# Kernel tuning notes

Hardware: AMD Instinct MI355X
Metric: run time of the kernel (lower is better)

Reference implementation:

```python
import jax, jax.numpy as jnp
import numpy as np

N = 100000   # num nodes
E = 1600000  # num edges
D = 64       # feature / hidden dim (irreps_in == hidden_dim)
SCALE = D ** -0.5


def setup_inputs() -> dict:
    key = jax.random.key(0)
    ks = jax.random.split(key, 6)
    x = jax.random.normal(ks[0], (N, D), dtype=jnp.float32)
    edge_index = jax.random.randint(ks[1], (2, E), 0, N, dtype=jnp.int32)
    std = D ** -0.5
    Wq = jax.random.normal(ks[2], (D, D), dtype=jnp.float32) * std
    Wk = jax.random.normal(ks[3], (D, D), dtype=jnp.float32) * std
    Wv = jax.random.normal(ks[4], (D, D), dtype=jnp.float32) * std
    Wo = jax.random.normal(ks[5], (D, D), dtype=jnp.float32) * std
    return {"x": x, "edge_index": edge_index, "Wq": Wq, "Wk": Wk, "Wv": Wv, "Wo": Wo}


def reference(x, edge_index, Wq, Wk, Wv, Wo):
    # Per-receiver variable-length attention over incoming neighbors.
    # Mathematically identical to the torch module's degree-bucketed SDPA
    # (softmax over each node's neighbor set), without padding buffers.
    sender, receiver = edge_index[0], edge_index[1]
    Q = x @ Wq  # [N, D]
    K = x @ Wk
    V = x @ Wv
    # per-edge logits: <Q[receiver], K[sender]> * scale
    s = jnp.einsum('ed,ed->e', Q[receiver], K[sender]) * SCALE  # [E]
    # numerically stable segment softmax over receiver groups
    m = jax.ops.segment_max(s, receiver, num_segments=N)  # -inf for empty segments
    m_safe = jnp.where(jnp.isfinite(m), m, 0.0)
    p = jnp.exp(s - m_safe[receiver])  # [E]
    denom = jax.ops.segment_sum(p, receiver, num_segments=N)  # [N]
    num = jax.ops.segment_sum(p[:, None] * V[sender], receiver, num_segments=N)  # [N, D]
    # zero-degree nodes get out = 0 (matches torch: skipped buckets + nan_to_num)
    out = jnp.where(denom[:, None] > 0,
                    num / jnp.maximum(denom, 1e-30)[:, None],
                    0.0)
    return x + out @ Wo
```

## Files before the change

kernel.cpp:

```cpp
#include <hip/hip_runtime.h>
#include <hip/hip_bf16.h>

#define DIM 64
#define SCALE 0.125f
#define BINSH 5
#define NPB 32
#define NBKT 8
#define SCAP 192
#define LLCAP (NBKT * SCAP)
#define CHUNK 16384
#define MAXBINS 3200

static __device__ __forceinline__ unsigned int pack2bf(float a, float b) {
    unsigned int ua = __float_as_uint(a), ub = __float_as_uint(b);
    ua += 0x7fffu + ((ua >> 16) & 1u);
    ub += 0x7fffu + ((ub >> 16) & 1u);
    return (ua >> 16) | (ub & 0xffff0000u);
}
static __device__ __forceinline__ float2 unpack2bf(unsigned int u) {
    return make_float2(__uint_as_float(u << 16), __uint_as_float(u & 0xffff0000u));
}

__global__ __launch_bounds__(1024) void k_prep(const int* __restrict__ send,
                                               const int* __restrict__ recv,
                                               const float* __restrict__ Wv,
                                               const float* __restrict__ Wo,
                                               float* __restrict__ Wvo,
                                               int* __restrict__ binCur,
                                               unsigned int* __restrict__ ebuf,
                                               int E, int NBK) {
    __shared__ __align__(16) float smem[8192];
    int* hist = (int*)smem;
    int* lcur = hist + MAXBINS;
    int tid = threadIdx.x;

    if (blockIdx.x == 0) {
        float* av = smem;
        float* bo = smem + 4096;
        ((float4*)av)[tid] = ((const float4*)Wv)[tid];
        ((float4*)bo)[tid] = ((const float4*)Wo)[tid];
        __syncthreads();
        int r = tid >> 4, c0 = (tid & 15) * 4;
        float acc[4] = {0.f, 0.f, 0.f, 0.f};
        for (int k = 0; k < 64; k++) {
            float a = av[r * 64 + k];
#pragma unroll
            for (int j = 0; j < 4; j++) acc[j] = fmaf(a, bo[k * 64 + c0 + j], acc[j]);
        }
#pragma unroll
        for (int j = 0; j < 4; j++) Wvo[r * 64 + c0 + j] = acc[j];
        __syncthreads();
    }

    int bucket = blockIdx.x & (NBKT - 1);
    int base = blockIdx.x * CHUNK;
    int lim = min(base + CHUNK, E);

    for (int i = tid; i < NBK; i += 1024) hist[i] = 0;
    __syncthreads();
    for (int i = base + tid; i < lim; i += 1024)
        atomicAdd(&hist[recv[i] >> BINSH], 1);
    __syncthreads();
    for (int i = tid; i < NBK; i += 1024) {
        int h = hist[i];
        lcur[i] = h ? atomicAdd(&binCur[i * NBKT + bucket], h) : 0;
    }
    __syncthreads();
    for (int i = base + tid; i < lim; i += 1024) {
        int r = recv[i];
        int b = r >> BINSH;
        int p = atomicAdd(&lcur[b], 1);
        if (p < SCAP)
            ebuf[((size_t)b * NBKT + bucket) * SCAP + p] =
                (unsigned)send[i] | ((unsigned)(r & (NPB - 1)) << 17);
    }
}

__global__ __launch_bounds__(256) void k_qkv(const float* __restrict__ x,
                                             const float* __restrict__ Wq,
                                             const float* __restrict__ Wk,
                                             const float* __restrict__ Wvo,
                                             float* __restrict__ Q,
                                             unsigned int* __restrict__ KVb,
                                             int N, int nchunk) {
    __shared__ __align__(16) float ws[64 * 64];
    __shared__ __align__(16) float xs[4][64 * 64];
    int tid = threadIdx.x;
    int wv = tid >> 6;
    int lane = tid & 63;
    int m = blockIdx.x / nchunk;
    int cb = blockIdx.x % nchunk;
    const float* W = (m == 0) ? Wq : ((m == 1) ? Wk : Wvo);

    for (int i = tid; i < 1024; i += 256) ((float4*)ws)[i] = ((const float4*)W)[i];
    __syncthreads();

    int base = cb * 256 + wv * 64;
    if (base < N) {
        float* xw = xs[wv];
#pragma unroll
        for (int c4 = 0; c4 < 16; c4++) {
            float4 v = make_float4(0.f, 0.f, 0.f, 0.f);
            if (base + lane < N) v = ((const float4*)x)[(size_t)(base + lane) * 16 + c4];
            xw[(c4 * 4 + 0) * 64 + lane] = v.x;
            xw[(c4 * 4 + 1) * 64 + lane] = v.y;
            xw[(c4 * 4 + 2) * 64 + lane] = v.z;
            xw[(c4 * 4 + 3) * 64 + lane] = v.w;
        }
        asm volatile("s_waitcnt lgkmcnt(0)" ::: "memory");

        int lr = lane >> 3;
        int lc = lane & 7;
        const float* xp = xw + lr * 8;
        const float* wp = ws + lc * 8;

        float acc[8][8];
#pragma unroll
        for (int i = 0; i < 8; i++)
#pragma unroll
            for (int j = 0; j < 8; j++) acc[i][j] = 0.f;

        float4 xa = *(const float4*)(xp);
        float4 xb = *(const float4*)(xp + 4);
        float4 wa = *(const float4*)(wp);
        float4 wb = *(const float4*)(wp + 4);
#pragma unroll 4
        for (int k = 0; k < 64; k++) {
            float4 xan, xbn, wan, wbn;
            if (k < 63) {
                xan = *(const float4*)(xp + (k + 1) * 64);
                xbn = *(const float4*)(xp + (k + 1) * 64 + 4);
                wan = *(const float4*)(wp + (k + 1) * 64);
                wbn = *(const float4*)(wp + (k + 1) * 64 + 4);
            }
            float xv[8] = {xa.x, xa.y, xa.z, xa.w, xb.x, xb.y, xb.z, xb.w};
            float wc[8] = {wa.x, wa.y, wa.z, wa.w, wb.x, wb.y, wb.z, wb.w};
#pragma unroll
            for (int i = 0; i < 8; i++)
#pragma unroll
                for (int j = 0; j < 8; j++)
                    acc[i][j] = fmaf(xv[i], wc[j], acc[i][j]);
            xa = xan; xb = xbn; wa = wan; wb = wbn;
        }

#pragma unroll
        for (int i = 0; i < 8; i++) {
            int row = base + lr * 8 + i;
            if (row < N) {
                if (m == 0) {
                    float* dst = &Q[(size_t)row * 64 + lc * 8];
                    ((float4*)dst)[0] = make_float4(acc[i][0], acc[i][1], acc[i][2], acc[i][3]);
                    ((float4*)dst)[1] = make_float4(acc[i][4], acc[i][5], acc[i][6], acc[i][7]);
                } else {
                    unsigned int* dst = &KVb[(size_t)row * 64 + (m - 1) * 32 + lc * 4];
                    uint4 pk;
                    pk.x = pack2bf(acc[i][0], acc[i][1]);
                    pk.y = pack2bf(acc[i][2], acc[i][3]);
                    pk.z = pack2bf(acc[i][4], acc[i][5]);
                    pk.w = pack2bf(acc[i][6], acc[i][7]);
                    *((uint4*)dst) = pk;
                }
            }
        }
    }
}

__global__ __launch_bounds__(256) void k_attn(const float* __restrict__ Q,
                                              const unsigned int* __restrict__ KVb,
                                              const float* __restrict__ x,
                                              const int* __restrict__ binCur,
                                              const unsigned int* __restrict__ ebuf,
                                              float* __restrict__ out, int N) {
    __shared__ unsigned int llist[LLCAP];
    __shared__ int ldeg[NPB], lofs[NPB + 1], lcur[NPB];
    __shared__ int segc[NBKT];
    int tid = threadIdx.x;
    int wv = tid >> 6;
    int lane = tid & 63;
    int g = lane >> 3;
    int sub = lane & 7;

    int j = blockIdx.x;
    const unsigned int* ebin = ebuf + (size_t)j * NBKT * SCAP;

    if (tid < NBKT) segc[tid] = min(binCur[j * NBKT + tid], SCAP);
    if (tid < NPB) ldeg[tid] = 0;
    __syncthreads();

    for (int s = 0; s < NBKT; s++) {
        int c = segc[s];
        for (int i = tid; i < c; i += 256)
            atomicAdd(&ldeg[(ebin[s * SCAP + i] >> 17) & (NPB - 1)], 1);
    }
    __syncthreads();

    if (wv == 0 && lane < NPB) {
        int d = ldeg[lane];
        int s = d;
        for (int o = 1; o < NPB; o <<= 1) {
            int t = __shfl_up(s, o, NPB);
            if ((lane & (NPB - 1)) >= o) s += t;
        }
        lofs[lane + 1] = s;
        lcur[lane] = s - d;
        if (lane == 0) lofs[0] = 0;
    }
    __syncthreads();

    for (int s = 0; s < NBKT; s++) {
        int c = segc[s];
        for (int i = tid; i < c; i += 256) {
            unsigned int u = ebin[s * SCAP + i];
            int n = (u >> 17) & (NPB - 1);
            int p = atomicAdd(&lcur[n], 1);
            llist[p] = u & 0x1FFFFu;
        }
    }
    __syncthreads();

    for (int n = wv; n < NPB; n += 4) {
        int r = (j << BINSH) + n;
        if (r >= N) break;
        int start = lofs[n];
        int end = lofs[n + 1];
        float4 qa = *((const float4*)&Q[(size_t)r * 64 + sub * 8]);
        float4 qb = *((const float4*)&Q[(size_t)r * 64 + sub * 8 + 4]);
        float q[8] = {qa.x, qa.y, qa.z, qa.w, qb.x, qb.y, qb.z, qb.w};
        float acc[8] = {0.f, 0.f, 0.f, 0.f, 0.f, 0.f, 0.f, 0.f};
        float dpart = 0.f;

        int eA = start + g;
        bool vA = eA < end;
        unsigned int sA = vA ? llist[eA] : 0u;
        uint4 kA = *((const uint4*)&KVb[(size_t)sA * 64 + sub * 4]);
        uint4 uA = *((const uint4*)&KVb[(size_t)sA * 64 + 32 + sub * 4]);
        int eB = start + 8 + g;
        bool vB = eB < end;
        unsigned int sB = vB ? llist[eB] : 0u;
        uint4 kB = *((const uint4*)&KVb[(size_t)sB * 64 + sub * 4]);
        uint4 uB = *((const uint4*)&KVb[(size_t)sB * 64 + 32 + sub * 4]);
        int eC = start + 16 + g;
        bool vC = eC < end;
        unsigned int sC = vC ? llist[eC] : 0u;
        uint4 kC = *((const uint4*)&KVb[(size_t)sC * 64 + sub * 4]);
        uint4 uC = *((const uint4*)&KVb[(size_t)sC * 64 + 32 + sub * 4]);

        for (int bb = start; bb < end; bb += 8) {
            int eD = bb + 24 + g;
            bool vD = eD < end;
            unsigned int sD = vD ? llist[eD] : 0u;
            uint4 kD = *((const uint4*)&KVb[(size_t)sD * 64 + sub * 4]);
            uint4 uD = *((const uint4*)&KVb[(size_t)sD * 64 + 32 + sub * 4]);

            float2 k01 = unpack2bf(kA.x), k23 = unpack2bf(kA.y);
            float2 k45 = unpack2bf(kA.z), k67 = unpack2bf(kA.w);
            float dot = q[0] * k01.x + q[1] * k01.y + q[2] * k23.x + q[3] * k23.y
                      + q[4] * k45.x + q[5] * k45.y + q[6] * k67.x + q[7] * k67.y;
            dot += __shfl_xor(dot, 1);
            dot += __shfl_xor(dot, 2);
            dot += __shfl_xor(dot, 4);
            float w = vA ? __expf(dot * SCALE) : 0.f;

            float2 v01 = unpack2bf(uA.x), v23 = unpack2bf(uA.y);
            float2 v45 = unpack2bf(uA.z), v67 = unpack2bf(uA.w);
            acc[0] = fmaf(w, v01.x, acc[0]);
            acc[1] = fmaf(w, v01.y, acc[1]);
            acc[2] = fmaf(w, v23.x, acc[2]);
            acc[3] = fmaf(w, v23.y, acc[3]);
            acc[4] = fmaf(w, v45.x, acc[4]);
            acc[5] = fmaf(w, v45.y, acc[5]);
            acc[6] = fmaf(w, v67.x, acc[6]);
            acc[7] = fmaf(w, v67.y, acc[7]);
            dpart += w;

            kA = kB; uA = uB; vA = vB;
            kB = kC; uB = uC; vB = vC;
            kC = kD; uC = uD; vC = vD;
        }

        dpart += __shfl_xor(dpart, 8); dpart += __shfl_xor(dpart, 16); dpart += __shfl_xor(dpart, 32);
#pragma unroll
        for (int jj = 0; jj < 8; jj++) {
            acc[jj] += __shfl_xor(acc[jj], 8);
            acc[jj] += __shfl_xor(acc[jj], 16);
            acc[jj] += __shfl_xor(acc[jj], 32);
        }

        float inv = (dpart > 0.f) ? (1.0f / dpart) : 0.f;

        if (g == 0) {
            float4 xa = *((const float4*)&x[(size_t)r * 64 + sub * 8]);
            float4 xb = *((const float4*)&x[(size_t)r * 64 + sub * 8 + 4]);
            float4 oa = make_float4(fmaf(acc[0], inv, xa.x), fmaf(acc[1], inv, xa.y),
                                    fmaf(acc[2], inv, xa.z), fmaf(acc[3], inv, xa.w));
            float4 ob = make_float4(fmaf(acc[4], inv, xb.x), fmaf(acc[5], inv, xb.y),
                                    fmaf(acc[6], inv, xb.z), fmaf(acc[7], inv, xb.w));
            *((float4*)&out[(size_t)r * 64 + sub * 8]) = oa;
            *((float4*)&out[(size_t)r * 64 + sub * 8 + 4]) = ob;
        }
    }
}


extern "C" void kernel_launch(void* const* d_in, const int* in_sizes, int n_in,
                              void* d_out, int out_size, void* d_ws, size_t ws_size,
                              hipStream_t stream) {
    const float* x  = (const float*)d_in[0];
    const int* edge = (const int*)d_in[1];
    const float* Wq = (const float*)d_in[2];
    const float* Wk = (const float*)d_in[3];
    const float* Wv = (const float*)d_in[4];
    const float* Wo = (const float*)d_in[5];
    float* out = (float*)d_out;

    int N = in_sizes[0] / DIM;
    int E = in_sizes[1] / 2;
    int NBK = (N + NPB - 1) >> BINSH;

    char* p = (char*)d_ws;
    auto cv = [&](size_t bytes) {
        char* r = p;
        p += ((bytes + 255) / 256) * 256;
        return r;
    };
    float*        Q      = (float*)cv((size_t)N * 64 * 4);
    unsigned int* KVb    = (unsigned int*)cv((size_t)N * 64 * 4);
    float*        Wvo    = (float*)cv(64 * 64 * 4);
    int*          binCur = (int*)cv((size_t)NBK * NBKT * 4);
    unsigned int* ebuf   = (unsigned int*)cv((size_t)NBK * NBKT * SCAP * 4);
    (void)ws_size; (void)n_in; (void)out_size;

    const int* send = edge;
    const int* recv = edge + E;

    hipMemsetAsync(binCur, 0, (size_t)NBK * NBKT * 4, stream);
    k_prep<<<(E + CHUNK - 1) / CHUNK, 1024, 0, stream>>>(send, recv, Wv, Wo, Wvo,
                                                         binCur, ebuf, E, NBK);
    int nchunk = (N + 255) / 256;
    k_qkv<<<3 * nchunk, 256, 0, stream>>>(x, Wq, Wk, Wvo, Q, KVb, N, nchunk);
    k_attn<<<NBK, 256, 0, stream>>>(Q, KVb, x, binCur, ebuf, out, N);
}
```

Baseline: 239.4 us.

## Process flat edge list per block with shared-memory atomic accumulation per receiver

Replaces the per-block counting sort of edges by receiver (degree histogram, prefix scan, scatter) with a flat concatenation of the bin segments. Waves now walk edge groups uniformly and accumulate weighted V rows and denominators into shared memory with atomics, indexed by receiver. Q rows for the block are staged in LDS. This removes two atomic passes and the per-node load imbalance across waves, at the cost of many LDS float atomics per edge and a cap of 768 edges per block, down from 1536.

```diff
diff --git a/kernel.cpp b/kernel.cpp
--- a/kernel.cpp
+++ b/kernel.cpp
@@ -7,7 +7,8 @@
 #define NPB 32
 #define NBKT 8
 #define SCAP 192
-#define LLCAP (NBKT * SCAP)
+#define LLCAP 768
+#define QS_S 68
 #define CHUNK 16384
 #define MAXBINS 3200
 
@@ -172,8 +173,11 @@
                                               const unsigned int* __restrict__ ebuf,
                                               float* __restrict__ out, int N) {
     __shared__ unsigned int llist[LLCAP];
-    __shared__ int ldeg[NPB], lofs[NPB + 1], lcur[NPB];
-    __shared__ int segc[NBKT];
+    __shared__ __align__(16) float qs[NPB * QS_S];
+    __shared__ __align__(16) float accw[NPB * QS_S];
+    __shared__ float dsum[NPB];
+    __shared__ int pref[NBKT + 1];
+
     int tid = threadIdx.x;
     int wv = tid >> 6;
     int lane = tid & 63;
@@ -183,120 +187,113 @@
     int j = blockIdx.x;
     const unsigned int* ebin = ebuf + (size_t)j * NBKT * SCAP;
 
-    if (tid < NBKT) segc[tid] = min(binCur[j * NBKT + tid], SCAP);
-    if (tid < NPB) ldeg[tid] = 0;
-    __syncthreads();
-
-    for (int s = 0; s < NBKT; s++) {
-        int c = segc[s];
-        for (int i = tid; i < c; i += 256)
-            atomicAdd(&ldeg[(ebin[s * SCAP + i] >> 17) & (NPB - 1)], 1);
-    }
-    __syncthreads();
-
-    if (wv == 0 && lane < NPB) {
-        int d = ldeg[lane];
-        int s = d;
-        for (int o = 1; o < NPB; o <<= 1) {
-            int t = __shfl_up(s, o, NPB);
-            if ((lane & (NPB - 1)) >= o) s += t;
-        }
-        lofs[lane + 1] = s;
-        lcur[lane] = s - d;
-        if (lane == 0) lofs[0] = 0;
-    }
-    __syncthreads();
-
-    for (int s = 0; s < NBKT; s++) {
-        int c = segc[s];
-        for (int i = tid; i < c; i += 256) {
-            unsigned int u = ebin[s * SCAP + i];
-            int n = (u >> 17) & (NPB - 1);
-            int p = atomicAdd(&lcur[n], 1);
-            llist[p] = u & 0x1FFFFu;
-        }
-    }
-    __syncthreads();
-
-    for (int n = wv; n < NPB; n += 4) {
+    for (int i = tid; i < NPB * 16; i += 256) {
+        int n = i >> 4, c4 = i & 15;
         int r = (j << BINSH) + n;
-        if (r >= N) break;
-        int start = lofs[n];
-        int end = lofs[n + 1];
-        float4 qa = *((const float4*)&Q[(size_t)r * 64 + sub * 8]);
-        float4 qb = *((const float4*)&Q[(size_t)r * 64 + sub * 8 + 4]);
-        float q[8] = {qa.x, qa.y, qa.z, qa.w, qb.x, qb.y, qb.z, qb.w};
-        float acc[8] = {0.f, 0.f, 0.f, 0.f, 0.f, 0.f, 0.f, 0.f};
-        float dpart = 0.f;
-
-        int eA = start + g;
-        bool vA = eA < end;
-        unsigned int sA = vA ? llist[eA] : 0u;
-        uint4 kA = *((const uint4*)&KVb[(size_t)sA * 64 + sub * 4]);
-        uint4 uA = *((const uint4*)&KVb[(size_t)sA * 64 + 32 + sub * 4]);
-        int eB = start + 8 + g;
-        bool vB = eB < end;
-        unsigned int sB = vB ? llist[eB] : 0u;
-        uint4 kB = *((const uint4*)&KVb[(size_t)sB * 64 + sub * 4]);
-        uint4 uB = *((const uint4*)&KVb[(size_t)sB * 64 + 32 + sub * 4]);
-        int eC = start + 16 + g;
-        bool vC = eC < end;
-        unsigned int sC = vC ? llist[eC] : 0u;
+        float4 v = make_float4(0.f, 0.f, 0.f, 0.f);
+        if (r < N) v = ((const float4*)Q)[(size_t)r * 16 + c4];
+        *(float4*)&qs[n * QS_S + c4 * 4] = v;
+    }
+    for (int i = tid; i < NPB * (QS_S / 4); i += 256)
+        *(float4*)&accw[i * 4] = make_float4(0.f, 0.f, 0.f, 0.f);
+    if (tid < NPB) dsum[tid] = 0.f;
+    if (tid < NBKT) pref[tid + 1] = min(binCur[j * NBKT + tid], SCAP);
+    __syncthreads();
+    if (tid == 0) {
+        int a = 0;
+        pref[0] = 0;
+#pragma unroll
+        for (int s = 0; s < NBKT; s++) {
+            a += pref[s + 1];
+            if (a > LLCAP) a = LLCAP;
+            pref[s + 1] = a;
+        }
+    }
+    __syncthreads();
+    int cnt = pref[NBKT];
+
+    for (int f = tid; f < cnt; f += 256) {
+        int s = 0;
+        while (f >= pref[s + 1]) s++;
+        llist[f] = ebin[s * SCAP + (f - pref[s])];
+    }
+    __syncthreads();
+
+    int nb = (cnt + 7) >> 3;
+
+    unsigned wA, wB, wC;
+    bool vA, vB, vC;
+    uint4 kA, uA, kB, uB;
+    {
+        int f = (wv << 3) + g;          vA = f < cnt; wA = vA ? llist[f] : 0u;
+        f = ((wv + 4) << 3) + g;        vB = f < cnt; wB = vB ? llist[f] : 0u;
+        f = ((wv + 8) << 3) + g;        vC = f < cnt; wC = vC ? llist[f] : 0u;
+    }
+    {
+        unsigned sA = wA & 0x1FFFFu, sB = wB & 0x1FFFFu;
+        kA = *((const uint4*)&KVb[(size_t)sA * 64 + sub * 4]);
+        uA = *((const uint4*)&KVb[(size_t)sA * 64 + 32 + sub * 4]);
+        kB = *((const uint4*)&KVb[(size_t)sB * 64 + sub * 4]);
+        uB = *((const uint4*)&KVb[(size_t)sB * 64 + 32 + sub * 4]);
+    }
+
+    for (int b = wv; b < nb; b += 4) {
+        int fD = ((b + 12) << 3) + g;
+        bool vD = fD < cnt;
+        unsigned wD = vD ? llist[fD] : 0u;
+        unsigned sC = wC & 0x1FFFFu;
         uint4 kC = *((const uint4*)&KVb[(size_t)sC * 64 + sub * 4]);
         uint4 uC = *((const uint4*)&KVb[(size_t)sC * 64 + 32 + sub * 4]);
 
-        for (int bb = start; bb < end; bb += 8) {
-            int eD = bb + 24 + g;
-            bool vD = eD < end;
-            unsigned int sD = vD ? llist[eD] : 0u;
-            uint4 kD = *((const uint4*)&KVb[(size_t)sD * 64 + sub * 4]);
-            uint4 uD = *((const uint4*)&KVb[(size_t)sD * 64 + 32 + sub * 4]);
-
-            float2 k01 = unpack2bf(kA.x), k23 = unpack2bf(kA.y);
-            float2 k45 = unpack2bf(kA.z), k67 = unpack2bf(kA.w);
-            float dot = q[0] * k01.x + q[1] * k01.y + q[2] * k23.x + q[3] * k23.y
-                      + q[4] * k45.x + q[5] * k45.y + q[6] * k67.x + q[7] * k67.y;
-            dot += __shfl_xor(dot, 1);
-            dot += __shfl_xor(dot, 2);
-            dot += __shfl_xor(dot, 4);
-            float w = vA ? __expf(dot * SCALE) : 0.f;
-
-            float2 v01 = unpack2bf(uA.x), v23 = unpack2bf(uA.y);
-            float2 v45 = unpack2bf(uA.z), v67 = unpack2bf(uA.w);
-            acc[0] = fmaf(w, v01.x, acc[0]);
-            acc[1] = fmaf(w, v01.y, acc[1]);
-            acc[2] = fmaf(w, v23.x, acc[2]);
-            acc[3] = fmaf(w, v23.y, acc[3]);
-            acc[4] = fmaf(w, v45.x, acc[4]);
-            acc[5] = fmaf(w, v45.y, acc[5]);
-            acc[6] = fmaf(w, v67.x, acc[6]);
-            acc[7] = fmaf(w, v67.y, acc[7]);
-            dpart += w;
-
-            kA = kB; uA = uB; vA = vB;
-            kB = kC; uB = uC; vB = vC;
-            kC = kD; uC = uD; vC = vD;
-        }
-
-        dpart += __shfl_xor(dpart, 8); dpart += __shfl_xor(dpart, 16); dpart += __shfl_xor(dpart, 32);
-#pragma unroll
-        for (int jj = 0; jj < 8; jj++) {
-            acc[jj] += __shfl_xor(acc[jj], 8);
-            acc[jj] += __shfl_xor(acc[jj], 16);
-            acc[jj] += __shfl_xor(acc[jj], 32);
-        }
-
-        float inv = (dpart > 0.f) ? (1.0f / dpart) : 0.f;
-
-        if (g == 0) {
-            float4 xa = *((const float4*)&x[(size_t)r * 64 + sub * 8]);
-            float4 xb = *((const float4*)&x[(size_t)r * 64 + sub * 8 + 4]);
-            float4 oa = make_float4(fmaf(acc[0], inv, xa.x), fmaf(acc[1], inv, xa.y),
-                                    fmaf(acc[2], inv, xa.z), fmaf(acc[3], inv, xa.w));
-            float4 ob = make_float4(fmaf(acc[4], inv, xb.x), fmaf(acc[5], inv, xb.y),
-                                    fmaf(acc[6], inv, xb.z), fmaf(acc[7], inv, xb.w));
-            *((float4*)&out[(size_t)r * 64 + sub * 8]) = oa;
-            *((float4*)&out[(size_t)r * 64 + sub * 8 + 4]) = ob;
+        int nA = (wA >> 17) & (NPB - 1);
+        const float* qp = &qs[nA * QS_S + sub * 8];
+        float4 qa = *(const float4*)qp;
+        float4 qb = *(const float4*)(qp + 4);
+        float2 k01 = unpack2bf(kA.x), k23 = unpack2bf(kA.y);
+        float2 k45 = unpack2bf(kA.z), k67 = unpack2bf(kA.w);
+        float dot = qa.x * k01.x + qa.y * k01.y + qa.z * k23.x + qa.w * k23.y
+                  + qb.x * k45.x + qb.y * k45.y + qb.z * k67.x + qb.w * k67.y;
+        dot += __shfl_xor(dot, 1);
+        dot += __shfl_xor(dot, 2);
+        dot += __shfl_xor(dot, 4);
+        float w = vA ? __expf(dot * SCALE) : 0.f;
+
+        float2 v01 = unpack2bf(uA.x), v23 = unpack2bf(uA.y);
+        float2 v45 = unpack2bf(uA.z), v67 = unpack2bf(uA.w);
+        float* ap = &accw[nA * QS_S + sub * 8];
+        atomicAdd(ap + 0, w * v01.x);
+        atomicAdd(ap + 1, w * v01.y);
+        atomicAdd(ap + 2, w * v23.x);
+        atomicAdd(ap + 3, w * v23.y);
+        atomicAdd(ap + 4, w * v45.x);
+        atomicAdd(ap + 5, w * v45.y);
+        atomicAdd(ap + 6, w * v67.x);
+        atomicAdd(ap + 7, w * v67.y);
+        if (sub == 0) atomicAdd(&dsum[nA], w);
+
+        wA = wB; vA = vB; kA = kB; uA = uB;
+        wB = wC; vB = vC; kB = kC; uB = uC;
+        wC = wD; vC = vD;
+    }
+    __syncthreads();
+
+    {
+        int n = tid >> 3;
+        int d0 = (tid & 7) * 8;
+        int r = (j << BINSH) + n;
+        if (r < N) {
+            float den = dsum[n];
+            float inv = (den > 0.f) ? (1.0f / den) : 0.f;
+            float4 a1 = *(const float4*)&accw[n * QS_S + d0];
+            float4 a2 = *(const float4*)&accw[n * QS_S + d0 + 4];
+            float4 xa = *((const float4*)&x[(size_t)r * 64 + d0]);
+            float4 xb = *((const float4*)&x[(size_t)r * 64 + d0 + 4]);
+            float4 oa = make_float4(fmaf(a1.x, inv, xa.x), fmaf(a1.y, inv, xa.y),
+                                    fmaf(a1.z, inv, xa.z), fmaf(a1.w, inv, xa.w));
+            float4 ob = make_float4(fmaf(a2.x, inv, xb.x), fmaf(a2.y, inv, xb.y),
+                                    fmaf(a2.z, inv, xb.z), fmaf(a2.w, inv, xb.w));
+            *((float4*)&out[(size_t)r * 64 + d0]) = oa;
+            *((float4*)&out[(size_t)r * 64 + d0 + 4]) = ob;
         }
     }
 }
```

New measurement: 741.3 us. 210% more time.

## Flatten per-wave edge batches across nodes to keep gather prefetch pipeline continuous

Applied to the files above, without the earlier changes.

Each wave now builds a queue of 8-edge batches covering all of its assigned nodes, and runs one continuous software-pipelined loop over that queue, flushing accumulators whenever the node changes. Before, the prefetch pipeline restarted for every node. Q rows are staged in shared memory up front, the bin scans become flat loops, the local list shrinks to 768 entries with clamping, and zero-degree nodes are written as plain x copies. The intent is to remove pipeline ramp-up and drain bubbles at node boundaries and to hide gather latency better. The cost is extra shared memory, per-batch shared-memory lookups, and the risk of silently dropping edges when a bin exceeds the list or queue capacity.

```diff
diff --git a/kernel.cpp b/kernel.cpp
--- a/kernel.cpp
+++ b/kernel.cpp
@@ -7,7 +7,9 @@
 #define NPB 32
 #define NBKT 8
 #define SCAP 192
-#define LLCAP (NBKT * SCAP)
+#define LLCAP 768
+#define QS_S 68
+#define WQCAP 112
 #define CHUNK 16384
 #define MAXBINS 3200
 
@@ -172,8 +174,12 @@
                                               const unsigned int* __restrict__ ebuf,
                                               float* __restrict__ out, int N) {
     __shared__ unsigned int llist[LLCAP];
+    __shared__ __align__(16) float qs[NPB * QS_S];
     __shared__ int ldeg[NPB], lofs[NPB + 1], lcur[NPB];
     __shared__ int segc[NBKT];
+    __shared__ unsigned short wbat[4][WQCAP];
+    __shared__ int wnbs[4];
+
     int tid = threadIdx.x;
     int wv = tid >> 6;
     int lane = tid & 63;
@@ -183,112 +189,100 @@
     int j = blockIdx.x;
     const unsigned int* ebin = ebuf + (size_t)j * NBKT * SCAP;
 
+    for (int i = tid; i < NPB * 16; i += 256) {
+        int n = i >> 4, c4 = i & 15;
+        int r = (j << BINSH) + n;
+        float4 v = make_float4(0.f, 0.f, 0.f, 0.f);
+        if (r < N) v = ((const float4*)Q)[(size_t)r * 16 + c4];
+        *(float4*)&qs[n * QS_S + c4 * 4] = v;
+    }
     if (tid < NBKT) segc[tid] = min(binCur[j * NBKT + tid], SCAP);
     if (tid < NPB) ldeg[tid] = 0;
     __syncthreads();
 
-    for (int s = 0; s < NBKT; s++) {
-        int c = segc[s];
-        for (int i = tid; i < c; i += 256)
-            atomicAdd(&ldeg[(ebin[s * SCAP + i] >> 17) & (NPB - 1)], 1);
+    for (int i = tid; i < NBKT * SCAP; i += 256) {
+        int s = i / SCAP;
+        if ((i - s * SCAP) < segc[s])
+            atomicAdd(&ldeg[(ebin[i] >> 17) & (NPB - 1)], 1);
     }
     __syncthreads();
 
     if (wv == 0 && lane < NPB) {
         int d = ldeg[lane];
-        int s = d;
+        int ssum = d;
         for (int o = 1; o < NPB; o <<= 1) {
-            int t = __shfl_up(s, o, NPB);
-            if ((lane & (NPB - 1)) >= o) s += t;
-        }
-        lofs[lane + 1] = s;
-        lcur[lane] = s - d;
+            int t = __shfl_up(ssum, o, NPB);
+            if (lane >= o) ssum += t;
+        }
+        lofs[lane + 1] = min(ssum, LLCAP);
+        lcur[lane] = min(ssum - d, LLCAP);
         if (lane == 0) lofs[0] = 0;
     }
     __syncthreads();
 
-    for (int s = 0; s < NBKT; s++) {
-        int c = segc[s];
-        for (int i = tid; i < c; i += 256) {
-            unsigned int u = ebin[s * SCAP + i];
+    for (int i = tid; i < NBKT * SCAP; i += 256) {
+        int s = i / SCAP;
+        if ((i - s * SCAP) < segc[s]) {
+            unsigned u = ebin[i];
             int n = (u >> 17) & (NPB - 1);
             int p = atomicAdd(&lcur[n], 1);
-            llist[p] = u & 0x1FFFFu;
-        }
-    }
-    __syncthreads();
-
-    for (int n = wv; n < NPB; n += 4) {
-        int r = (j << BINSH) + n;
-        if (r >= N) break;
-        int start = lofs[n];
-        int end = lofs[n + 1];
-        float4 qa = *((const float4*)&Q[(size_t)r * 64 + sub * 8]);
-        float4 qb = *((const float4*)&Q[(size_t)r * 64 + sub * 8 + 4]);
-        float q[8] = {qa.x, qa.y, qa.z, qa.w, qb.x, qb.y, qb.z, qb.w};
-        float acc[8] = {0.f, 0.f, 0.f, 0.f, 0.f, 0.f, 0.f, 0.f};
-        float dpart = 0.f;
-
-        int eA = start + g;
-        bool vA = eA < end;
-        unsigned int sA = vA ? llist[eA] : 0u;
-        uint4 kA = *((const uint4*)&KVb[(size_t)sA * 64 + sub * 4]);
-        uint4 uA = *((const uint4*)&KVb[(size_t)sA * 64 + 32 + sub * 4]);
-        int eB = start + 8 + g;
-        bool vB = eB < end;
-        unsigned int sB = vB ? llist[eB] : 0u;
-        uint4 kB = *((const uint4*)&KVb[(size_t)sB * 64 + sub * 4]);
-        uint4 uB = *((const uint4*)&KVb[(size_t)sB * 64 + 32 + sub * 4]);
-        int eC = start + 16 + g;
-        bool vC = eC < end;
-        unsigned int sC = vC ? llist[eC] : 0u;
-        uint4 kC = *((const uint4*)&KVb[(size_t)sC * 64 + sub * 4]);
-        uint4 uC = *((const uint4*)&KVb[(size_t)sC * 64 + 32 + sub * 4]);
-
-        for (int bb = start; bb < end; bb += 8) {
-            int eD = bb + 24 + g;
-            bool vD = eD < end;
-            unsigned int sD = vD ? llist[eD] : 0u;
-            uint4 kD = *((const uint4*)&KVb[(size_t)sD * 64 + sub * 4]);
-            uint4 uD = *((const uint4*)&KVb[(size_t)sD * 64 + 32 + sub * 4]);
-
-            float2 k01 = unpack2bf(kA.x), k23 = unpack2bf(kA.y);
-            float2 k45 = unpack2bf(kA.z), k67 = unpack2bf(kA.w);
-            float dot = q[0] * k01.x + q[1] * k01.y + q[2] * k23.x + q[3] * k23.y
-                      + q[4] * k45.x + q[5] * k45.y + q[6] * k67.x + q[7] * k67.y;
-            dot += __shfl_xor(dot, 1);
-            dot += __shfl_xor(dot, 2);
-            dot += __shfl_xor(dot, 4);
-            float w = vA ? __expf(dot * SCALE) : 0.f;
-
-            float2 v01 = unpack2bf(uA.x), v23 = unpack2bf(uA.y);
-            float2 v45 = unpack2bf(uA.z), v67 = unpack2bf(uA.w);
-            acc[0] = fmaf(w, v01.x, acc[0]);
-            acc[1] = fmaf(w, v01.y, acc[1]);
-            acc[2] = fmaf(w, v23.x, acc[2]);
-            acc[3] = fmaf(w, v23.y, acc[3]);
-            acc[4] = fmaf(w, v45.x, acc[4]);
-            acc[5] = fmaf(w, v45.y, acc[5]);
-            acc[6] = fmaf(w, v67.x, acc[6]);
-            acc[7] = fmaf(w, v67.y, acc[7]);
-            dpart += w;
-
-            kA = kB; uA = uB; vA = vB;
-            kB = kC; uB = uC; vB = vC;
-            kC = kD; uC = uD; vC = vD;
-        }
-
-        dpart += __shfl_xor(dpart, 8); dpart += __shfl_xor(dpart, 16); dpart += __shfl_xor(dpart, 32);
+            if (p < LLCAP) llist[p] = u & 0x1FFFFu;
+        }
+    }
+    if (lane == 0) {
+        int c = 0;
+        for (int i = 0; i < 8; i++) {
+            int n = wv + 4 * i;
+            int deg = lofs[n + 1] - lofs[n];
+            int nb = (deg + 7) >> 3;
+            for (int t = 0; t < nb && c < WQCAP; t++)
+                wbat[wv][c++] = (unsigned short)(n | (t << 5));
+        }
+        wnbs[wv] = c;
+    }
+    __syncthreads();
+
+    int wnb = wnbs[wv];
+    const unsigned short* wq = wbat[wv];
+
+    int n0 = 0, n1 = 0;
+    bool v0 = false, v1 = false;
+    unsigned s0 = 0, s1 = 0;
+    if (0 < wnb) {
+        unsigned short w = wq[0];
+        n0 = w & 31; int t = w >> 5;
+        int e = lofs[n0] + (t << 3) + g;
+        v0 = e < lofs[n0 + 1];
+        s0 = v0 ? llist[e] : 0u;
+    }
+    if (1 < wnb) {
+        unsigned short w = wq[1];
+        n1 = w & 31; int t = w >> 5;
+        int e = lofs[n1] + (t << 3) + g;
+        v1 = e < lofs[n1 + 1];
+        s1 = v1 ? llist[e] : 0u;
+    }
+    uint4 k0 = *((const uint4*)&KVb[(size_t)s0 * 64 + sub * 4]);
+    uint4 u0 = *((const uint4*)&KVb[(size_t)s0 * 64 + 32 + sub * 4]);
+    uint4 k1 = *((const uint4*)&KVb[(size_t)s1 * 64 + sub * 4]);
+    uint4 u1 = *((const uint4*)&KVb[(size_t)s1 * 64 + 32 + sub * 4]);
+
+    int curn = -1;
+    float acc[8] = {0.f, 0.f, 0.f, 0.f, 0.f, 0.f, 0.f, 0.f};
+    float dp = 0.f;
+
+    auto flushnode = [&](int n) {
+        float d = dp;
+        d += __shfl_xor(d, 8); d += __shfl_xor(d, 16); d += __shfl_xor(d, 32);
 #pragma unroll
         for (int jj = 0; jj < 8; jj++) {
             acc[jj] += __shfl_xor(acc[jj], 8);
             acc[jj] += __shfl_xor(acc[jj], 16);
             acc[jj] += __shfl_xor(acc[jj], 32);
         }
-
-        float inv = (dpart > 0.f) ? (1.0f / dpart) : 0.f;
-
+        float inv = (d > 0.f) ? (1.0f / d) : 0.f;
         if (g == 0) {
+            int r = (j << BINSH) + n;
             float4 xa = *((const float4*)&x[(size_t)r * 64 + sub * 8]);
             float4 xb = *((const float4*)&x[(size_t)r * 64 + sub * 8 + 4]);
             float4 oa = make_float4(fmaf(acc[0], inv, xa.x), fmaf(acc[1], inv, xa.y),
@@ -298,6 +292,63 @@
             *((float4*)&out[(size_t)r * 64 + sub * 8]) = oa;
             *((float4*)&out[(size_t)r * 64 + sub * 8 + 4]) = ob;
         }
+    };
+
+    for (int p = 0; p < wnb; p++) {
+        int n2 = 0; bool v2 = false; unsigned s2 = 0;
+        if (p + 2 < wnb) {
+            unsigned short w = wq[p + 2];
+            n2 = w & 31; int t = w >> 5;
+            int e = lofs[n2] + (t << 3) + g;
+            v2 = e < lofs[n2 + 1];
+            s2 = v2 ? llist[e] : 0u;
+        }
+        uint4 k2 = *((const uint4*)&KVb[(size_t)s2 * 64 + sub * 4]);
+        uint4 u2 = *((const uint4*)&KVb[(size_t)s2 * 64 + 32 + sub * 4]);
+
+        if (n0 != curn) {
+            if (curn >= 0) flushnode(curn);
+            curn = n0;
+#pragma unroll
+            for (int jj = 0; jj < 8; jj++) acc[jj] = 0.f;
+            dp = 0.f;
+        }
+
+        const float* qp = &qs[n0 * QS_S + sub * 8];
+        float4 qa = *(const float4*)qp;
+        float4 qb = *(const float4*)(qp + 4);
+        float2 k01 = unpack2bf(k0.x), k23 = unpack2bf(k0.y);
+        float2 k45 = unpack2bf(k0.z), k67 = unpack2bf(k0.w);
+        float dot = qa.x * k01.x + qa.y * k01.y + qa.z * k23.x + qa.w * k23.y
+                  + qb.x * k45.x + qb.y * k45.y + qb.z * k67.x + qb.w * k67.y;
+        dot += __shfl_xor(dot, 1);
+        dot += __shfl_xor(dot, 2);
+        dot += __shfl_xor(dot, 4);
+        float w = v0 ? __expf(dot * SCALE) : 0.f;
+
+        float2 v01 = unpack2bf(u0.x), v23 = unpack2bf(u0.y);
+        float2 v45 = unpack2bf(u0.z), v67 = unpack2bf(u0.w);
+        acc[0] = fmaf(w, v01.x, acc[0]);
+        acc[1] = fmaf(w, v01.y, acc[1]);
+        acc[2] = fmaf(w, v23.x, acc[2]);
+        acc[3] = fmaf(w, v23.y, acc[3]);
+        acc[4] = fmaf(w, v45.x, acc[4]);
+        acc[5] = fmaf(w, v45.y, acc[5]);
+        acc[6] = fmaf(w, v67.x, acc[6]);
+        acc[7] = fmaf(w, v67.y, acc[7]);
+        dp += w;
+
+        n0 = n1; v0 = v1; k0 = k1; u0 = u1;
+        n1 = n2; v1 = v2; k1 = k2; u1 = u2;
+    }
+    if (curn >= 0) flushnode(curn);
+
+#pragma unroll
+    for (int i = 0; i < 8; i++) {
+        int n = wv + 4 * i;
+        int r = (j << BINSH) + n;
+        if (r < N && lofs[n + 1] == lofs[n])
+            out[(size_t)r * 64 + lane] = x[(size_t)r * 64 + lane];
     }
 }
 
```

Measured after the change: 254.5 us. 6.3% more time.
